# Performance work log

Hardware: AMD Instinct MI355X
Metric: run time of the kernel (lower is better)

## Reference

```python
import jax, jax.numpy as jnp
import numpy as np

EMBED = 1024
HEADS = 16
HEAD_DIM = EMBED // HEADS


def setup_inputs() -> dict:
    key = jax.random.key(0)
    ks = jax.random.split(key, 6)
    scale = 1.0 / np.sqrt(EMBED)
    x = jax.random.normal(ks[0], (2, 2048, EMBED), dtype=jnp.float32)
    # nn.Linear weights stored as [out_features, in_features]
    Wq = jax.random.normal(ks[1], (EMBED, EMBED), dtype=jnp.float32) * scale
    Wk = jax.random.normal(ks[2], (EMBED, EMBED), dtype=jnp.float32) * scale
    Wv = jax.random.normal(ks[3], (EMBED, EMBED), dtype=jnp.float32) * scale
    Wo = jax.random.normal(ks[4], (EMBED, EMBED), dtype=jnp.float32) * scale
    bo = jax.random.normal(ks[5], (EMBED,), dtype=jnp.float32) * scale
    return {"x": x, "Wq": Wq, "Wk": Wk, "Wv": Wv, "Wo": Wo, "bo": bo}


def reference(x, Wq, Wk, Wv, Wo, bo):
    N, L, E = x.shape
    # projections (torch Linear: x @ W.T)
    q = (x @ Wq.T).reshape(N, L, HEADS, HEAD_DIM).transpose(0, 2, 1, 3)  # [N,H,L,D]
    k = (x @ Wk.T).reshape(N, L, HEADS, HEAD_DIM).transpose(0, 2, 1, 3)
    v = (x @ Wv.T).reshape(N, L, HEADS, HEAD_DIM).transpose(0, 2, 1, 3)
    # scores scaled by sqrt(embed_size) (as in source, not sqrt(head_dim))
    scores = jnp.einsum("nhqd,nhkd->nhqk", q, k) / jnp.sqrt(jnp.float32(E))
    attn = jax.nn.softmax(scores, axis=-1)
    out = jnp.einsum("nhqk,nhkd->nhqd", attn, v)  # [N,H,L,D]
    out = out.transpose(0, 2, 1, 3).reshape(N, L, E)
    return out @ Wo.T + bo
```

## Files before the change

### kernel.cpp

```cpp
#include <hip/hip_runtime.h>
#include <hip/hip_bf16.h>

constexpr int NB  = 2;
constexpr int SL  = 2048;
constexpr int EMB = 1024;
constexpr int NH  = 16;
constexpr int HD  = 64;
constexpr int MT  = NB * SL;
constexpr size_t PROJ = (size_t)MT * EMB;

typedef __attribute__((ext_vector_type(8))) short bf16x8;
typedef __attribute__((ext_vector_type(4))) float f32x4;

__device__ inline short f2b(float f) {
  __hip_bfloat16 b = __float2bfloat16(f);
  short s; __builtin_memcpy(&s, &b, 2); return s;
}

#define GLDS16(g, l)                                                     \
  __builtin_amdgcn_global_load_lds(                                      \
      (const __attribute__((address_space(1))) void*)(g),                \
      (__attribute__((address_space(3))) void*)(l), 16, 0, 0)

__global__ __launch_bounds__(256) void cast_all(
    const float* __restrict__ x,  const float* __restrict__ wq,
    const float* __restrict__ wk, const float* __restrict__ wv,
    const float* __restrict__ wo, short* __restrict__ xb,
    short* __restrict__ wqkv, short* __restrict__ wob) {
  const size_t t = (size_t)blockIdx.x * 256 + threadIdx.x;
  const float* src; short* dst; size_t base;
  if (t < 1048576)      { src = x;  dst = xb;              base = 0; }
  else if (t < 1310720) { src = wq; dst = wqkv;            base = 1048576; }
  else if (t < 1572864) { src = wk; dst = wqkv + (1 << 20); base = 1310720; }
  else if (t < 1835008) { src = wv; dst = wqkv + (2 << 20); base = 1572864; }
  else                  { src = wo; dst = wob;             base = 1835008; }
  const size_t i = t - base;
  const float4 v = ((const float4*)src)[i];
  const short4 o = {f2b(v.x), f2b(v.y), f2b(v.z), f2b(v.w)};
  ((short4*)dst)[i] = o;
}

__global__ __launch_bounds__(256) void gemm_qkv(
    const short* __restrict__ A, const short* __restrict__ W,
    short* __restrict__ qb, short* __restrict__ kb, short* __restrict__ vt) {
  __shared__ short As[128 * 32];
  __shared__ short Bs[128 * 32];
  const int tid = threadIdx.x;
  const int w = tid >> 6, lane = tid & 63;
  const int la = lane >> 4, lb = lane & 15;
  const int wm = w & 1, wn = w >> 1;
  const int m0 = blockIdx.y << 7, n0 = blockIdx.x << 7;
  const int srow = lane >> 2, scol = (lane & 3) << 3;
  const short* a0 = A + (size_t)(m0 + w * 16 + srow) * 1024 + scol;
  const short* b0 = W + (size_t)(n0 + w * 16 + srow) * 1024 + scol;
  short* lA0 = As + (w * 16) * 32;
  short* lA1 = As + (64 + w * 16) * 32;
  short* lB0 = Bs + (w * 16) * 32;
  short* lB1 = Bs + (64 + w * 16) * 32;

  f32x4 acc[4][4];
#pragma unroll
  for (int i = 0; i < 4; ++i)
#pragma unroll
    for (int j = 0; j < 4; ++j) acc[i][j] = (f32x4){0.f, 0.f, 0.f, 0.f};

  for (int k0 = 0; k0 < 1024; k0 += 32) {
    __syncthreads();
    GLDS16(a0 + k0, lA0);
    GLDS16(a0 + 64 * 1024 + k0, lA1);
    GLDS16(b0 + k0, lB0);
    GLDS16(b0 + 64 * 1024 + k0, lB1);
    __syncthreads();
    bf16x8 af[4], bfr[4];
#pragma unroll
    for (int i = 0; i < 4; ++i)
      af[i] = *(const bf16x8*)&As[(wm * 64 + i * 16 + lb) * 32 + la * 8];
#pragma unroll
    for (int j = 0; j < 4; ++j)
      bfr[j] = *(const bf16x8*)&Bs[(wn * 64 + j * 16 + lb) * 32 + la * 8];
#pragma unroll
    for (int i = 0; i < 4; ++i)
#pragma unroll
      for (int j = 0; j < 4; ++j)
        acc[i][j] = __builtin_amdgcn_mfma_f32_16x16x32_bf16(af[i], bfr[j],
                                                            acc[i][j], 0, 0, 0);
  }

  const int region = n0 >> 10;
  if (region == 0) {
    const float sc = 0.03125f * 1.44269504f;
#pragma unroll
    for (int j = 0; j < 4; ++j) {
      const int nj = (n0 & 1023) + wn * 64 + j * 16 + lb;
#pragma unroll
      for (int i = 0; i < 4; ++i) {
        const int mi = m0 + wm * 64 + i * 16 + la * 4;
#pragma unroll
        for (int r = 0; r < 4; ++r)
          qb[(size_t)(mi + r) * 1024 + nj] = f2b(acc[i][j][r] * sc);
      }
    }
  } else if (region == 1) {
#pragma unroll
    for (int j = 0; j < 4; ++j) {
      const int nj = (n0 & 1023) + wn * 64 + j * 16 + lb;
      const int hh = nj >> 6, d = nj & 63;
      const int ks = d >> 5, Gd = (d >> 3) & 3, jj = d & 7;
#pragma unroll
      for (int i = 0; i < 4; ++i) {
        const int mi = m0 + wm * 64 + i * 16 + la * 4;
        const int nbi = mi >> 11, seq = mi & (SL - 1);
        const size_t base = ((size_t)(nbi * NH + hh) << 17) +
                            (size_t)(seq >> 4) * 1024 + ks * 512 + Gd * 128 +
                            (seq & 15) * 8 + jj;
#pragma unroll
        for (int r = 0; r < 4; ++r) kb[base + r * 8] = f2b(acc[i][j][r]);
      }
    }
  } else {
#pragma unroll
    for (int j = 0; j < 4; ++j) {
      const int nv = (n0 - 2048) + wn * 64 + j * 16 + lb;
      const int hh = nv >> 6, d = nv & 63;
      const int mtd = d >> 4, lbv = d & 15;
#pragma unroll
      for (int i = 0; i < 4; ++i) {
        const int mi = m0 + wm * 64 + i * 16 + la * 4;
        const int nbi = mi >> 11, seq = mi & (SL - 1);
        const int kq = seq >> 5, g = (seq >> 2) & 3, hi = (seq >> 4) & 1;
        const short4 o = {f2b(acc[i][j][0]), f2b(acc[i][j][1]),
                          f2b(acc[i][j][2]), f2b(acc[i][j][3])};
        *(short4*)&vt[((size_t)(nbi * NH + hh) << 17) + (size_t)kq * 2048 +
                      mtd * 512 + g * 128 + lbv * 8 + 4 * hi] = o;
      }
    }
  }
}

__global__ __launch_bounds__(256) void gemm_out(
    const short* __restrict__ A, const short* __restrict__ W,
    const float* __restrict__ bias, float* __restrict__ out) {
  __shared__ short As[128 * 32];
  __shared__ short Bs[64 * 32];
  const int tid = threadIdx.x;
  const int w = tid >> 6, lane = tid & 63;
  const int la = lane >> 4, lb = lane & 15;
  const int wm = w & 1, wn = w >> 1;
  const int m0 = blockIdx.y << 7, n0 = blockIdx.x << 6;
  const int srow = lane >> 2, scol = (lane & 3) << 3;
  const short* a0 = A + (size_t)(m0 + w * 16 + srow) * 1024 + scol;
  const short* b0 = W + (size_t)(n0 + w * 16 + srow) * 1024 + scol;
  short* lA0 = As + (w * 16) * 32;
  short* lA1 = As + (64 + w * 16) * 32;
  short* lB0 = Bs + (w * 16) * 32;

  f32x4 acc[4][2];
#pragma unroll
  for (int i = 0; i < 4; ++i)
#pragma unroll
    for (int j = 0; j < 2; ++j) acc[i][j] = (f32x4){0.f, 0.f, 0.f, 0.f};

  for (int k0 = 0; k0 < 1024; k0 += 32) {
    __syncthreads();
    GLDS16(a0 + k0, lA0);
    GLDS16(a0 + 64 * 1024 + k0, lA1);
    GLDS16(b0 + k0, lB0);
    __syncthreads();
    bf16x8 af[4], bfr[2];
#pragma unroll
    for (int i = 0; i < 4; ++i)
      af[i] = *(const bf16x8*)&As[(wm * 64 + i * 16 + lb) * 32 + la * 8];
#pragma unroll
    for (int j = 0; j < 2; ++j)
      bfr[j] = *(const bf16x8*)&Bs[(wn * 32 + j * 16 + lb) * 32 + la * 8];
#pragma unroll
    for (int i = 0; i < 4; ++i)
#pragma unroll
      for (int j = 0; j < 2; ++j)
        acc[i][j] = __builtin_amdgcn_mfma_f32_16x16x32_bf16(af[i], bfr[j],
                                                            acc[i][j], 0, 0, 0);
  }
#pragma unroll
  for (int j = 0; j < 2; ++j) {
    const int nj = n0 + wn * 32 + j * 16 + lb;
    const float bv = bias[nj];
#pragma unroll
    for (int i = 0; i < 4; ++i) {
      const int mi = m0 + wm * 64 + i * 16 + la * 4;
#pragma unroll
      for (int r = 0; r < 4; ++r)
        out[(size_t)(mi + r) * 1024 + nj] = acc[i][j][r] + bv;
    }
  }
}

#define LOADK(DK, KB32)                                                      \
  do {                                                                       \
    _Pragma("unroll") for (int rr_ = 0; rr_ < 2; ++rr_)                      \
        _Pragma("unroll") for (int ks_ = 0; ks_ < 2; ++ks_)                  \
            DK[rr_][ks_] = *(const bf16x8*)(Kb + (size_t)(KB32) * 2048 +     \
                                            rr_ * 1024 + ks_ * 512);         \
  } while (0)

#define LOADV(DV, KB32)                                                      \
  do {                                                                       \
    _Pragma("unroll") for (int md_ = 0; md_ < 4; ++md_)                      \
        DV[md_] = *(const bf16x8*)(Vb + (size_t)(KB32) * 2048 + md_ * 512);  \
  } while (0)

#define ATTN_STEP(AK, AV)                                                    \
  do {                                                                       \
    f32x4 S[2][4];                                                           \
    _Pragma("unroll") for (int mt = 0; mt < 2; ++mt)                         \
        _Pragma("unroll") for (int nt = 0; nt < 4; ++nt)                     \
            S[mt][nt] = (f32x4){0.f, 0.f, 0.f, 0.f};                         \
    _Pragma("unroll") for (int ks = 0; ks < 2; ++ks)                         \
        _Pragma("unroll") for (int nt = 0; nt < 4; ++nt) {                   \
      S[0][nt] = __builtin_amdgcn_mfma_f32_16x16x32_bf16(AK[0][ks],          \
                     bQ[nt][ks], S[0][nt], 0, 0, 0);                         \
      S[1][nt] = __builtin_amdgcn_mfma_f32_16x16x32_bf16(AK[1][ks],          \
                     bQ[nt][ks], S[1][nt], 0, 0, 0);                         \
    }                                                                        \
    _Pragma("unroll") for (int nt = 0; nt < 4; ++nt) {                       \
      _Pragma("unroll") for (int mt = 0; mt < 2; ++mt)                       \
          _Pragma("unroll") for (int r = 0; r < 4; ++r) {                    \
        const float p = __builtin_amdgcn_exp2f(S[mt][nt][r]);                \
        S[mt][nt][r] = p;                                                    \
        lacc[nt] += p;                                                       \
      }                                                                      \
      bf16x8 B2;                                                             \
      B2[0] = f2b(S[0][nt][0]); B2[1] = f2b(S[0][nt][1]);                    \
      B2[2] = f2b(S[0][nt][2]); B2[3] = f2b(S[0][nt][3]);                    \
      B2[4] = f2b(S[1][nt][0]); B2[5] = f2b(S[1][nt][1]);                    \
      B2[6] = f2b(S[1][nt][2]); B2[7] = f2b(S[1][nt][3]);                    \
      _Pragma("unroll") for (int mtd = 0; mtd < 4; ++mtd)                    \
          O[mtd][nt] = __builtin_amdgcn_mfma_f32_16x16x32_bf16(              \
              AV[mtd], B2, O[mtd][nt], 0, 0, 0);                             \
    }                                                                        \
  } while (0)

__global__ __launch_bounds__(256, 2) void attn_mfma(const short* __restrict__ Qg,
                                                    const short* __restrict__ Kp,
                                                    const short* __restrict__ Vp,
                                                    short* __restrict__ Ab) {
  __shared__ __align__(16) float red[2][64][68];
  __shared__ float lred[128];
  const int tid = threadIdx.x;
  const int w = tid >> 6, lane = tid & 63;
  const int G = lane >> 4, lb = lane & 15;
  const int wk = w & 1, wq = w >> 1;
  const int h = blockIdx.x, qt = blockIdx.y, n = blockIdx.z;

  const short* Qb = Qg + ((size_t)(n * SL + (qt << 7) + 64 * wq)) * EMB + h * HD;
  bf16x8 bQ[4][2];
#pragma unroll
  for (int nt = 0; nt < 4; ++nt)
#pragma unroll
    for (int ks = 0; ks < 2; ++ks)
      bQ[nt][ks] =
          *(const bf16x8*)(Qb + (size_t)(16 * nt + lb) * EMB + 32 * ks + 8 * G);

  f32x4 O[4][4];
  float lacc[4] = {0.f, 0.f, 0.f, 0.f};
#pragma unroll
  for (int i = 0; i < 4; ++i)
#pragma unroll
    for (int j = 0; j < 4; ++j) O[i][j] = (f32x4){0.f, 0.f, 0.f, 0.f};

  const short* Kb = Kp + (((size_t)(n * NH + h)) << 17) + lane * 8;
  const short* Vb = Vp + (((size_t)(n * NH + h)) << 17) + lane * 8;

  bf16x8 K0[2][2], V0[4], K1[2][2], V1[4];
  LOADK(K0, 2 * wk);
  LOADV(V0, 2 * wk);
  for (int it = 0; it < 32; it += 2) {
    const int kA = 2 * it + 2 * wk;
    LOADK(K1, kA + 1);
    LOADV(V1, kA + 1);
    ATTN_STEP(K0, V0);
    if (it + 2 < 32) {
      LOADK(K0, kA + 4);
      LOADV(V0, kA + 4);
    }
    ATTN_STEP(K1, V1);
  }

#pragma unroll
  for (int nt = 0; nt < 4; ++nt) {
    lacc[nt] += __shfl_xor(lacc[nt], 16);
    lacc[nt] += __shfl_xor(lacc[nt], 32);
  }

  if (wk == 1) {
#pragma unroll
    for (int nt = 0; nt < 4; ++nt) {
      const int q = 16 * nt + lb;
#pragma unroll
      for (int mtd = 0; mtd < 4; ++mtd)
        *(f32x4*)&red[wq][q][16 * mtd + 4 * G] = O[mtd][nt];
      if (G == 0) lred[wq * 64 + q] = lacc[nt];
    }
  }
  __syncthreads();
  if (wk == 0) {
    short* Ao = Ab + ((size_t)(n * SL + (qt << 7) + 64 * wq)) * EMB + h * HD;
#pragma unroll
    for (int nt = 0; nt < 4; ++nt) {
      const int q = 16 * nt + lb;
      const float inv = 1.f / (lacc[nt] + lred[wq * 64 + q]);
#pragma unroll
      for (int mtd = 0; mtd < 4; ++mtd) {
        const f32x4 t = *(const f32x4*)&red[wq][q][16 * mtd + 4 * G];
        const f32x4 s = t + O[mtd][nt];
        const short4 o = {f2b(s[0] * inv), f2b(s[1] * inv), f2b(s[2] * inv),
                          f2b(s[3] * inv)};
        *(short4*)(Ao + (size_t)q * EMB + 16 * mtd + 4 * G) = o;
      }
    }
  }
}

extern "C" void kernel_launch(void* const* d_in, const int* in_sizes, int n_in,
                              void* d_out, int out_size, void* d_ws, size_t ws_size,
                              hipStream_t stream) {
  const float* x  = (const float*)d_in[0];
  const float* Wq = (const float*)d_in[1];
  const float* Wk = (const float*)d_in[2];
  const float* Wv = (const float*)d_in[3];
  const float* Wo = (const float*)d_in[4];
  const float* bo = (const float*)d_in[5];
  float* out = (float*)d_out;

  short* xb   = (short*)d_ws;
  short* wqkv = xb + PROJ;
  short* wob  = wqkv + 3u * EMB * EMB;
  short* qb   = wob + (size_t)EMB * EMB;
  short* kb   = qb + PROJ;
  short* vt   = kb + PROJ;
  short* ab   = qb;

  cast_all<<<8192, 256, 0, stream>>>(x, Wq, Wk, Wv, Wo, xb, wqkv, wob);
  gemm_qkv<<<dim3(24, 32), 256, 0, stream>>>(xb, wqkv, qb, kb, vt);
  attn_mfma<<<dim3(NH, SL / 128, NB), 256, 0, stream>>>(qb, kb, vt, ab);
  gemm_out<<<dim3(16, 32), 256, 0, stream>>>(ab, wob, bo, out);
}
```

Baseline: 175.5 us.

## Double GEMM K-tile to 64 with XOR-swizzled LDS and raise MFMA wave priority

Both GEMM kernels now stage K-tiles of 64 instead of 32. This halves the number of barrier pairs per K loop and issues more global-to-LDS loads per sync. The LDS layout uses an XOR swizzle of the 16-byte column chunk by row to avoid bank conflicts on the MFMA fragment reads, and LDS use per block doubles. Separately, the attention step wraps its MFMA bursts in s_setprio(1)/s_setprio(0) so the wave doing matrix math gets scheduling priority over waves doing exp and conversion work.

```diff
diff --git a/kernel.cpp b/kernel.cpp
--- a/kernel.cpp
+++ b/kernel.cpp
@@ -43,20 +43,19 @@
 __global__ __launch_bounds__(256) void gemm_qkv(
     const short* __restrict__ A, const short* __restrict__ W,
     short* __restrict__ qb, short* __restrict__ kb, short* __restrict__ vt) {
-  __shared__ short As[128 * 32];
-  __shared__ short Bs[128 * 32];
+  __shared__ short As[128 * 64];
+  __shared__ short Bs[128 * 64];
   const int tid = threadIdx.x;
   const int w = tid >> 6, lane = tid & 63;
   const int la = lane >> 4, lb = lane & 15;
   const int wm = w & 1, wn = w >> 1;
   const int m0 = blockIdx.y << 7, n0 = blockIdx.x << 7;
-  const int srow = lane >> 2, scol = (lane & 3) << 3;
-  const short* a0 = A + (size_t)(m0 + w * 16 + srow) * 1024 + scol;
-  const short* b0 = W + (size_t)(n0 + w * 16 + srow) * 1024 + scol;
-  short* lA0 = As + (w * 16) * 32;
-  short* lA1 = As + (64 + w * 16) * 32;
-  short* lB0 = Bs + (w * 16) * 32;
-  short* lB1 = Bs + (64 + w * 16) * 32;
+  const int srow = lane >> 3;
+  const int scol = ((lane & 7) ^ srow) << 3;
+  const short* a0 = A + (size_t)(m0 + w * 32 + srow) * 1024 + scol;
+  const short* b0 = W + (size_t)(n0 + w * 32 + srow) * 1024 + scol;
+  short* lAw = As + (w * 32) * 64;
+  short* lBw = Bs + (w * 32) * 64;
 
   f32x4 acc[4][4];
 #pragma unroll
@@ -64,26 +63,33 @@
 #pragma unroll
     for (int j = 0; j < 4; ++j) acc[i][j] = (f32x4){0.f, 0.f, 0.f, 0.f};
 
-  for (int k0 = 0; k0 < 1024; k0 += 32) {
+  for (int k0 = 0; k0 < 1024; k0 += 64) {
     __syncthreads();
-    GLDS16(a0 + k0, lA0);
-    GLDS16(a0 + 64 * 1024 + k0, lA1);
-    GLDS16(b0 + k0, lB0);
-    GLDS16(b0 + 64 * 1024 + k0, lB1);
+#pragma unroll
+    for (int g = 0; g < 4; ++g) GLDS16(a0 + g * 8 * 1024 + k0, lAw + g * 8 * 64);
+#pragma unroll
+    for (int g = 0; g < 4; ++g) GLDS16(b0 + g * 8 * 1024 + k0, lBw + g * 8 * 64);
     __syncthreads();
-    bf16x8 af[4], bfr[4];
-#pragma unroll
-    for (int i = 0; i < 4; ++i)
-      af[i] = *(const bf16x8*)&As[(wm * 64 + i * 16 + lb) * 32 + la * 8];
-#pragma unroll
-    for (int j = 0; j < 4; ++j)
-      bfr[j] = *(const bf16x8*)&Bs[(wn * 64 + j * 16 + lb) * 32 + la * 8];
-#pragma unroll
-    for (int i = 0; i < 4; ++i)
-#pragma unroll
-      for (int j = 0; j < 4; ++j)
-        acc[i][j] = __builtin_amdgcn_mfma_f32_16x16x32_bf16(af[i], bfr[j],
-                                                            acc[i][j], 0, 0, 0);
+#pragma unroll
+    for (int ks = 0; ks < 2; ++ks) {
+      bf16x8 af[4], bfr[4];
+#pragma unroll
+      for (int i = 0; i < 4; ++i) {
+        const int row = wm * 64 + i * 16 + lb;
+        af[i] = *(const bf16x8*)&As[row * 64 + (((ks << 2) + la) ^ (row & 7)) * 8];
+      }
+#pragma unroll
+      for (int j = 0; j < 4; ++j) {
+        const int row = wn * 64 + j * 16 + lb;
+        bfr[j] = *(const bf16x8*)&Bs[row * 64 + (((ks << 2) + la) ^ (row & 7)) * 8];
+      }
+#pragma unroll
+      for (int i = 0; i < 4; ++i)
+#pragma unroll
+        for (int j = 0; j < 4; ++j)
+          acc[i][j] = __builtin_amdgcn_mfma_f32_16x16x32_bf16(af[i], bfr[j],
+                                                              acc[i][j], 0, 0, 0);
+    }
   }
 
   const int region = n0 >> 10;
@@ -140,19 +146,19 @@
 __global__ __launch_bounds__(256) void gemm_out(
     const short* __restrict__ A, const short* __restrict__ W,
     const float* __restrict__ bias, float* __restrict__ out) {
-  __shared__ short As[128 * 32];
-  __shared__ short Bs[64 * 32];
+  __shared__ short As[128 * 64];
+  __shared__ short Bs[64 * 64];
   const int tid = threadIdx.x;
   const int w = tid >> 6, lane = tid & 63;
   const int la = lane >> 4, lb = lane & 15;
   const int wm = w & 1, wn = w >> 1;
   const int m0 = blockIdx.y << 7, n0 = blockIdx.x << 6;
-  const int srow = lane >> 2, scol = (lane & 3) << 3;
-  const short* a0 = A + (size_t)(m0 + w * 16 + srow) * 1024 + scol;
+  const int srow = lane >> 3;
+  const int scol = ((lane & 7) ^ srow) << 3;
+  const short* a0 = A + (size_t)(m0 + w * 32 + srow) * 1024 + scol;
   const short* b0 = W + (size_t)(n0 + w * 16 + srow) * 1024 + scol;
-  short* lA0 = As + (w * 16) * 32;
-  short* lA1 = As + (64 + w * 16) * 32;
-  short* lB0 = Bs + (w * 16) * 32;
+  short* lAw = As + (w * 32) * 64;
+  short* lBw = Bs + (w * 16) * 64;
 
   f32x4 acc[4][2];
 #pragma unroll
@@ -160,25 +166,33 @@
 #pragma unroll
     for (int j = 0; j < 2; ++j) acc[i][j] = (f32x4){0.f, 0.f, 0.f, 0.f};
 
-  for (int k0 = 0; k0 < 1024; k0 += 32) {
+  for (int k0 = 0; k0 < 1024; k0 += 64) {
     __syncthreads();
-    GLDS16(a0 + k0, lA0);
-    GLDS16(a0 + 64 * 1024 + k0, lA1);
-    GLDS16(b0 + k0, lB0);
+#pragma unroll
+    for (int g = 0; g < 4; ++g) GLDS16(a0 + g * 8 * 1024 + k0, lAw + g * 8 * 64);
+#pragma unroll
+    for (int g = 0; g < 2; ++g) GLDS16(b0 + g * 8 * 1024 + k0, lBw + g * 8 * 64);
     __syncthreads();
-    bf16x8 af[4], bfr[2];
-#pragma unroll
-    for (int i = 0; i < 4; ++i)
-      af[i] = *(const bf16x8*)&As[(wm * 64 + i * 16 + lb) * 32 + la * 8];
-#pragma unroll
-    for (int j = 0; j < 2; ++j)
-      bfr[j] = *(const bf16x8*)&Bs[(wn * 32 + j * 16 + lb) * 32 + la * 8];
-#pragma unroll
-    for (int i = 0; i < 4; ++i)
-#pragma unroll
-      for (int j = 0; j < 2; ++j)
-        acc[i][j] = __builtin_amdgcn_mfma_f32_16x16x32_bf16(af[i], bfr[j],
-                                                            acc[i][j], 0, 0, 0);
+#pragma unroll
+    for (int ks = 0; ks < 2; ++ks) {
+      bf16x8 af[4], bfr[2];
+#pragma unroll
+      for (int i = 0; i < 4; ++i) {
+        const int row = wm * 64 + i * 16 + lb;
+        af[i] = *(const bf16x8*)&As[row * 64 + (((ks << 2) + la) ^ (row & 7)) * 8];
+      }
+#pragma unroll
+      for (int j = 0; j < 2; ++j) {
+        const int row = wn * 32 + j * 16 + lb;
+        bfr[j] = *(const bf16x8*)&Bs[row * 64 + (((ks << 2) + la) ^ (row & 7)) * 8];
+      }
+#pragma unroll
+      for (int i = 0; i < 4; ++i)
+#pragma unroll
+        for (int j = 0; j < 2; ++j)
+          acc[i][j] = __builtin_amdgcn_mfma_f32_16x16x32_bf16(af[i], bfr[j],
+                                                              acc[i][j], 0, 0, 0);
+    }
   }
 #pragma unroll
   for (int j = 0; j < 2; ++j) {
@@ -214,6 +228,7 @@
     _Pragma("unroll") for (int mt = 0; mt < 2; ++mt)                         \
         _Pragma("unroll") for (int nt = 0; nt < 4; ++nt)                     \
             S[mt][nt] = (f32x4){0.f, 0.f, 0.f, 0.f};                         \
+    __builtin_amdgcn_s_setprio(1);                                           \
     _Pragma("unroll") for (int ks = 0; ks < 2; ++ks)                         \
         _Pragma("unroll") for (int nt = 0; nt < 4; ++nt) {                   \
       S[0][nt] = __builtin_amdgcn_mfma_f32_16x16x32_bf16(AK[0][ks],          \
@@ -221,6 +236,7 @@
       S[1][nt] = __builtin_amdgcn_mfma_f32_16x16x32_bf16(AK[1][ks],          \
                      bQ[nt][ks], S[1][nt], 0, 0, 0);                         \
     }                                                                        \
+    __builtin_amdgcn_s_setprio(0);                                           \
     _Pragma("unroll") for (int nt = 0; nt < 4; ++nt) {                       \
       _Pragma("unroll") for (int mt = 0; mt < 2; ++mt)                       \
           _Pragma("unroll") for (int r = 0; r < 4; ++r) {                    \
@@ -233,9 +249,11 @@
       B2[2] = f2b(S[0][nt][2]); B2[3] = f2b(S[0][nt][3]);                    \
       B2[4] = f2b(S[1][nt][0]); B2[5] = f2b(S[1][nt][1]);                    \
       B2[6] = f2b(S[1][nt][2]); B2[7] = f2b(S[1][nt][3]);                    \
+      __builtin_amdgcn_s_setprio(1);                                         \
       _Pragma("unroll") for (int mtd = 0; mtd < 4; ++mtd)                    \
           O[mtd][nt] = __builtin_amdgcn_mfma_f32_16x16x32_bf16(              \
               AV[mtd], B2, O[mtd][nt], 0, 0, 0);                             \
+      __builtin_amdgcn_s_setprio(0);                                         \
     }                                                                        \
   } while (0)
 
```

After: 174.0 us (median of 2 runs). About the same (-0.8%).
